# Optimization experiments

Measured on AMD Instinct MI355X. Metric: run time of the kernel, lower is better.

## Reference

```python
import jax, jax.numpy as jnp
import numpy as np

D_MODEL = 1024
H = 16
DK = D_MODEL // H
B, S = 2, 2048
NEG = -1e9


def setup_inputs() -> dict:
    key = jax.random.key(0)
    ks = jax.random.split(key, 7)
    scale = 1.0 / np.sqrt(D_MODEL)
    inp = {
        "q": jax.random.normal(ks[0], (B, S, D_MODEL), jnp.float32),
        "k": jax.random.normal(ks[1], (B, S, D_MODEL), jnp.float32),
        "v": jax.random.normal(ks[2], (B, S, D_MODEL), jnp.float32),
        # causal mask, broadcastable to (B, H, S, S); positions with 0 are masked
        "mask": jnp.tril(jnp.ones((S, S), dtype=bool))[None, None, :, :],
        "w_q": jax.random.normal(ks[3], (D_MODEL, D_MODEL), jnp.float32) * scale,
        "w_k": jax.random.normal(ks[4], (D_MODEL, D_MODEL), jnp.float32) * scale,
        "w_v": jax.random.normal(ks[5], (D_MODEL, D_MODEL), jnp.float32) * scale,
        "w_o": jax.random.normal(ks[6], (D_MODEL, D_MODEL), jnp.float32) * scale,
    }
    return inp


def reference(q, k, v, mask, w_q, w_k, w_v, w_o):
    # Linear projections (nn.Linear with bias=False: x @ W.T)
    query = q @ w_q.T  # (B, S, d_model)
    key_ = k @ w_k.T
    value = v @ w_v.T
    # split heads -> (B, h, S, dk)
    def split(x):
        return x.reshape(x.shape[0], x.shape[1], H, DK).transpose(0, 2, 1, 3)
    qh, kh, vh = split(query), split(key_), split(value)
    # scaled dot-product attention with full score materialization
    scores = jnp.einsum("bhqd,bhkd->bhqk", qh, kh) / jnp.sqrt(jnp.float32(DK))
    scores = jnp.where(mask, scores, NEG)
    attn = jax.nn.softmax(scores, axis=-1)  # (B, h, S, S); dropout p=0.0 -> identity
    out = jnp.einsum("bhqk,bhkd->bhqd", attn, vh)
    # merge heads -> (B, S, d_model)
    out = out.transpose(0, 2, 1, 3).reshape(out.shape[0], -1, H * DK)
    return out @ w_o.T
```

## Files before the change

kernel.cpp:

```cpp
#include <hip/hip_runtime.h>
#include <cstdint>
#include <cstddef>

typedef __bf16 bf16;
typedef __attribute__((ext_vector_type(4))) __bf16 bf16x4;
typedef __attribute__((ext_vector_type(8))) __bf16 bf16x8;
typedef __attribute__((ext_vector_type(4))) float floatx4;
typedef __attribute__((ext_vector_type(4))) short short4v;

#define MFMA16(a, b, c) __builtin_amdgcn_mfma_f32_16x16x32_bf16((a), (b), (c), 0, 0, 0)

__device__ __forceinline__ floatx4 MFMAK16(bf16x4 a, bf16x4 b, floatx4 c) {
#if __has_builtin(__builtin_amdgcn_mfma_f32_16x16x16bf16_1k)
  return __builtin_amdgcn_mfma_f32_16x16x16bf16_1k(
      __builtin_bit_cast(short4v, a), __builtin_bit_cast(short4v, b), c, 0, 0, 0);
#else
  floatx4 d;
  asm("v_mfma_f32_16x16x16_bf16 %0, %1, %2, %3"
      : "=v"(d)
      : "v"(a), "v"(b), "v"(c));
  return d;
#endif
}

constexpr int DMODEL = 1024;
constexpr int NH = 16;
constexpr int DKH = 64;
constexpr int B_ = 2;
constexpr int S_ = 2048;
constexpr int MTOT = B_ * S_;
constexpr float CEXP = 0.125f * 1.44269504f;

__device__ __forceinline__ void load_lds16(const void* g, void* l) {
  __builtin_amdgcn_global_load_lds(
      (const __attribute__((address_space(1))) uint32_t*)g,
      (__attribute__((address_space(3))) uint32_t*)l, 16, 0, 0);
}

__device__ __forceinline__ bf16x8 frag64(const bf16* lds, int row, int p) {
  int s = p ^ (row & 7);
  return *(const bf16x8*)&lds[row * 64 + s * 8];
}
__device__ __forceinline__ bf16x4 frag64h(const bf16* lds, int row, int p, int h) {
  int s = p ^ (row & 7);
  return *(const bf16x4*)&lds[row * 64 + s * 8 + h * 4];
}

__device__ __forceinline__ void stage32_bf16(const bf16* __restrict__ src,
                                             bf16* lds, int wave, int lane,
                                             int ldg) {
#pragma unroll
  for (int i = 0; i < 2; ++i) {
    int cb = (wave * 2 + i) * 64;
    int c = cb + lane;
    int r = c >> 2;
    int s = (c & 3) ^ ((r >> 1) & 3);
    load_lds16(&src[(size_t)r * ldg + s * 8], &lds[cb * 8]);
  }
}
__device__ __forceinline__ bf16x8 frag32_bf16(const bf16* lds, int row,
                                              int quad) {
  int s = quad ^ ((row >> 1) & 3);
  return *(const bf16x8*)&lds[row * 32 + s * 8];
}
__device__ __forceinline__ void stage32_f32(const float* __restrict__ src,
                                            float* lds, int wave, int lane,
                                            int ldg) {
#pragma unroll
  for (int i = 0; i < 4; ++i) {
    int cb = (wave * 4 + i) * 64;
    int c = cb + lane;
    int r = c >> 3;
    int s = (c & 7) ^ (r & 7);
    load_lds16(&src[(size_t)r * ldg + s * 4], &lds[cb * 4]);
  }
}
__device__ __forceinline__ bf16x8 frag32_f32(const float* lds, int row,
                                             int quad) {
  int s1 = (2 * quad) ^ (row & 7);
  int s2 = (2 * quad + 1) ^ (row & 7);
  float4 a = *(const float4*)&lds[row * 32 + s1 * 4];
  float4 b = *(const float4*)&lds[row * 32 + s2 * 4];
  bf16x8 h = {(bf16)a.x, (bf16)a.y, (bf16)a.z, (bf16)a.w,
              (bf16)b.x, (bf16)b.y, (bf16)b.z, (bf16)b.w};
  return h;
}

__global__ __launch_bounds__(256) void convert_kernel(
    const float* __restrict__ q, const float* __restrict__ k,
    const float* __restrict__ v, const float* __restrict__ wq,
    const float* __restrict__ wk, const float* __restrict__ wv,
    const float* __restrict__ wo, bf16* __restrict__ qb, bf16* __restrict__ kb,
    bf16* __restrict__ vb, bf16* __restrict__ wqb, bf16* __restrict__ wkb,
    bf16* __restrict__ wvb, bf16* __restrict__ wob) {
  const float* src;
  bf16* dst;
  size_t n;
  switch (blockIdx.y) {
    case 0: src = q;  dst = qb;  n = (size_t)MTOT * DMODEL; break;
    case 1: src = k;  dst = kb;  n = (size_t)MTOT * DMODEL; break;
    case 2: src = v;  dst = vb;  n = (size_t)MTOT * DMODEL; break;
    case 3: src = wq; dst = wqb; n = (size_t)DMODEL * DMODEL; break;
    case 4: src = wk; dst = wkb; n = (size_t)DMODEL * DMODEL; break;
    case 5: src = wv; dst = wvb; n = (size_t)DMODEL * DMODEL; break;
    default: src = wo; dst = wob; n = (size_t)DMODEL * DMODEL; break;
  }
  size_t idx = ((size_t)blockIdx.x * 256 + threadIdx.x) * 8;
  if (idx >= n) return;
  float4 f0 = *(const float4*)&src[idx];
  float4 f1 = *(const float4*)&src[idx + 4];
  bf16x8 h = {(bf16)f0.x, (bf16)f0.y, (bf16)f0.z, (bf16)f0.w,
              (bf16)f1.x, (bf16)f1.y, (bf16)f1.z, (bf16)f1.w};
  *(bf16x8*)&dst[idx] = h;
}

template <typename TC>
__device__ __forceinline__ void gemm64(const bf16* __restrict__ A,
                                       const bf16* __restrict__ W,
                                       TC* __restrict__ C,
                                       bf16* __restrict__ vt, int K,
                                       int m0, int n0, float ascale) {
  constexpr int N = DMODEL;
  __shared__ alignas(16) bf16 As[128 * 64];
  __shared__ alignas(16) bf16 Bs[128 * 64];

  const int tid = threadIdx.x;
  const int wave = tid >> 6;
  const int lane = tid & 63;
  const int quad = lane >> 4;
  const int l16 = lane & 15;
  const int wm = (wave >> 1) * 64;
  const int wn = (wave & 1) * 64;

  floatx4 acc[4][4] = {};

  for (int k0 = 0; k0 < K; k0 += 64) {
#pragma unroll
    for (int i = 0; i < 4; ++i) {
      int cb = (wave * 4 + i) * 64;
      int c = cb + lane;
      int r = c >> 3;
      int s = (c & 7) ^ (r & 7);
      load_lds16(&A[(size_t)(m0 + r) * K + k0 + s * 8], &As[cb * 8]);
      load_lds16(&W[(size_t)(n0 + r) * K + k0 + s * 8], &Bs[cb * 8]);
    }
    __syncthreads();

#pragma unroll
    for (int kk = 0; kk < 2; ++kk) {
      bf16x8 af[4], bfv[4];
#pragma unroll
      for (int mi = 0; mi < 4; ++mi)
        af[mi] = frag64(As, wm + mi * 16 + l16, kk * 4 + quad);
#pragma unroll
      for (int ni = 0; ni < 4; ++ni)
        bfv[ni] = frag64(Bs, wn + ni * 16 + l16, kk * 4 + quad);
#pragma unroll
      for (int mi = 0; mi < 4; ++mi)
#pragma unroll
        for (int ni = 0; ni < 4; ++ni)
          acc[mi][ni] = MFMA16(af[mi], bfv[ni], acc[mi][ni]);
    }
    __syncthreads();
  }

  if (vt) {
#pragma unroll
    for (int mi = 0; mi < 4; ++mi)
#pragma unroll
      for (int ni = 0; ni < 4; ++ni)
#pragma unroll
        for (int r = 0; r < 4; ++r) {
          int row = m0 + wm + mi * 16 + quad * 4 + r;
          int col = n0 + wn + ni * 16 + l16;
          int bb = row >> 11, s = row & 2047;
          int h = col >> 6, d = col & 63;
          vt[(size_t)((bb * NH + h) * DKH + d) * S_ + s] = (bf16)acc[mi][ni][r];
        }
  } else {
#pragma unroll
    for (int mi = 0; mi < 4; ++mi)
#pragma unroll
      for (int ni = 0; ni < 4; ++ni)
#pragma unroll
        for (int r = 0; r < 4; ++r) {
          int row = m0 + wm + mi * 16 + quad * 4 + r;
          int col = n0 + wn + ni * 16 + l16;
          C[(size_t)row * N + col] = (TC)(acc[mi][ni][r] * ascale);
        }
  }
}

__global__ __launch_bounds__(256, 3) void qkv64_kernel(
    const bf16* __restrict__ q, const bf16* __restrict__ k,
    const bf16* __restrict__ v, const bf16* __restrict__ wq,
    const bf16* __restrict__ wk, const bf16* __restrict__ wv,
    bf16* __restrict__ Q, bf16* __restrict__ K, bf16* __restrict__ Vt) {
  const int bid = blockIdx.x;
  const int xcd = bid & 7;
  const int j = bid >> 3;
  const int n = j & 7;
  const int rowslot = j >> 3;
  const int p = xcd * 12 + rowslot;
  const int z = p >> 5;
  const int y = p & 31;

  const bf16* A = (z == 0) ? q : (z == 1) ? k : v;
  const bf16* W = (z == 0) ? wq : (z == 1) ? wk : wv;
  bf16* C = (z == 0) ? Q : K;
  gemm64<bf16>(A, W, (z == 2) ? nullptr : C, (z == 2) ? Vt : nullptr,
               DMODEL, y * 128, n * 128, (z == 0) ? CEXP : 1.0f);
}

__global__ __launch_bounds__(256) void oproj64_kernel(
    const bf16* __restrict__ A, const bf16* __restrict__ W,
    float* __restrict__ C) {
  constexpr int K = DMODEL;
  constexpr int N = DMODEL;
  __shared__ alignas(16) bf16 As[64 * 64];
  __shared__ alignas(16) bf16 Bs[128 * 64];

  const int bid = blockIdx.x;
  const int xcd = bid & 7;
  const int j = bid >> 3;
  const int n = j & 7;
  const int slot = j >> 3;
  const int mt = xcd * 8 + slot;
  const int m0 = mt * 64;
  const int n0 = n * 128;

  const int tid = threadIdx.x;
  const int wave = tid >> 6;
  const int lane = tid & 63;
  const int quad = lane >> 4;
  const int l16 = lane & 15;
  const int wm = (wave >> 1) * 32;
  const int wn = (wave & 1) * 64;

  floatx4 acc[2][4] = {};

  for (int k0 = 0; k0 < K; k0 += 64) {
#pragma unroll
    for (int i = 0; i < 2; ++i) {
      int cb = (wave * 2 + i) * 64;
      int c = cb + lane;
      int r = c >> 3;
      int s = (c & 7) ^ (r & 7);
      load_lds16(&A[(size_t)(m0 + r) * K + k0 + s * 8], &As[cb * 8]);
    }
#pragma unroll
    for (int i = 0; i < 4; ++i) {
      int cb = (wave * 4 + i) * 64;
      int c = cb + lane;
      int r = c >> 3;
      int s = (c & 7) ^ (r & 7);
      load_lds16(&W[(size_t)(n0 + r) * K + k0 + s * 8], &Bs[cb * 8]);
    }
    __syncthreads();

#pragma unroll
    for (int kk = 0; kk < 2; ++kk) {
      bf16x8 af[2], bfv[4];
#pragma unroll
      for (int mi = 0; mi < 2; ++mi)
        af[mi] = frag64(As, wm + mi * 16 + l16, kk * 4 + quad);
#pragma unroll
      for (int ni = 0; ni < 4; ++ni)
        bfv[ni] = frag64(Bs, wn + ni * 16 + l16, kk * 4 + quad);
#pragma unroll
      for (int mi = 0; mi < 2; ++mi)
#pragma unroll
        for (int ni = 0; ni < 4; ++ni)
          acc[mi][ni] = MFMA16(af[mi], bfv[ni], acc[mi][ni]);
    }
    __syncthreads();
  }

#pragma unroll
  for (int mi = 0; mi < 2; ++mi)
#pragma unroll
    for (int ni = 0; ni < 4; ++ni)
#pragma unroll
      for (int r = 0; r < 4; ++r) {
        int row = m0 + wm + mi * 16 + quad * 4 + r;
        int col = n0 + wn + ni * 16 + l16;
        C[(size_t)row * N + col] = acc[mi][ni][r];
      }
}

template <typename TA, typename TW, typename TC>
__device__ __forceinline__ void gemm_core(const TA* __restrict__ A,
                                          const TW* __restrict__ W,
                                          TC* __restrict__ C,
                                          bf16* __restrict__ vt, int K,
                                          int m0, int n0, float ascale) {
  constexpr int N = DMODEL;
  __shared__ alignas(16) char smem[128 * 32 * (sizeof(TA) + sizeof(TW))];
  TA* As = (TA*)smem;
  TW* Bs = (TW*)(smem + 128 * 32 * sizeof(TA));

  const int tid = threadIdx.x;
  const int wave = tid >> 6;
  const int lane = tid & 63;
  const int quad = lane >> 4;
  const int l16 = lane & 15;
  const int wm = (wave >> 1) * 64;
  const int wn = (wave & 1) * 64;

  floatx4 acc[4][4] = {};

  for (int k0 = 0; k0 < K; k0 += 32) {
    if constexpr (sizeof(TA) == 2)
      stage32_bf16((const bf16*)A + (size_t)m0 * K + k0, (bf16*)As, wave, lane, K);
    else
      stage32_f32((const float*)A + (size_t)m0 * K + k0, (float*)As, wave, lane, K);
    if constexpr (sizeof(TW) == 2)
      stage32_bf16((const bf16*)W + (size_t)n0 * K + k0, (bf16*)Bs, wave, lane, K);
    else
      stage32_f32((const float*)W + (size_t)n0 * K + k0, (float*)Bs, wave, lane, K);
    __syncthreads();

    bf16x8 af[4], bfv[4];
#pragma unroll
    for (int mi = 0; mi < 4; ++mi) {
      if constexpr (sizeof(TA) == 2)
        af[mi] = frag32_bf16((const bf16*)As, wm + mi * 16 + l16, quad);
      else
        af[mi] = frag32_f32((const float*)As, wm + mi * 16 + l16, quad);
    }
#pragma unroll
    for (int ni = 0; ni < 4; ++ni) {
      if constexpr (sizeof(TW) == 2)
        bfv[ni] = frag32_bf16((const bf16*)Bs, wn + ni * 16 + l16, quad);
      else
        bfv[ni] = frag32_f32((const float*)Bs, wn + ni * 16 + l16, quad);
    }
#pragma unroll
    for (int mi = 0; mi < 4; ++mi)
#pragma unroll
      for (int ni = 0; ni < 4; ++ni)
        acc[mi][ni] = MFMA16(af[mi], bfv[ni], acc[mi][ni]);
    __syncthreads();
  }

  if (vt) {
#pragma unroll
    for (int mi = 0; mi < 4; ++mi)
#pragma unroll
      for (int ni = 0; ni < 4; ++ni)
#pragma unroll
        for (int r = 0; r < 4; ++r) {
          int row = m0 + wm + mi * 16 + quad * 4 + r;
          int col = n0 + wn + ni * 16 + l16;
          int bb = row >> 11, s = row & 2047;
          int h = col >> 6, d = col & 63;
          vt[(size_t)((bb * NH + h) * DKH + d) * S_ + s] = (bf16)acc[mi][ni][r];
        }
  } else {
#pragma unroll
    for (int mi = 0; mi < 4; ++mi)
#pragma unroll
      for (int ni = 0; ni < 4; ++ni)
#pragma unroll
        for (int r = 0; r < 4; ++r) {
          int row = m0 + wm + mi * 16 + quad * 4 + r;
          int col = n0 + wn + ni * 16 + l16;
          C[(size_t)row * N + col] = (TC)(acc[mi][ni][r] * ascale);
        }
  }
}

__global__ __launch_bounds__(256) void qkv_f32_kernel(
    const float* __restrict__ q, const float* __restrict__ k,
    const float* __restrict__ v, const float* __restrict__ wq,
    const float* __restrict__ wk, const float* __restrict__ wv,
    bf16* __restrict__ Q, bf16* __restrict__ K, bf16* __restrict__ Vt) {
  const int bid = blockIdx.x;
  const int xcd = bid & 7;
  const int j = bid >> 3;
  const int n = j & 7;
  const int rowslot = j >> 3;
  const int p = xcd * 12 + rowslot;
  const int z = p >> 5;
  const int y = p & 31;
  const float* A = (z == 0) ? q : (z == 1) ? k : v;
  const float* W = (z == 0) ? wq : (z == 1) ? wk : wv;
  bf16* C = (z == 0) ? Q : K;
  gemm_core<float, float, bf16>(A, W, (z == 2) ? nullptr : C,
                                (z == 2) ? Vt : nullptr, DMODEL, y * 128,
                                n * 128, (z == 0) ? CEXP : 1.0f);
}

__global__ __launch_bounds__(256) void oproj_f32_kernel(
    const bf16* __restrict__ A, const float* __restrict__ W,
    float* __restrict__ C) {
  const int bid = blockIdx.x;
  const int xcd = bid & 7;
  const int j = bid >> 3;
  const int n = j & 7;
  const int rowslot = j >> 3;
  const int y = xcd * 4 + rowslot;
  gemm_core<bf16, float, float>(A, W, C, nullptr, DMODEL, y * 128, n * 128,
                                1.0f);
}

__global__ __launch_bounds__(256) void attn6_kernel(const bf16* __restrict__ Q,
                                                    const bf16* __restrict__ K,
                                                    const bf16* __restrict__ Vt,
                                                    bf16* __restrict__ O) {
  __shared__ alignas(16) bf16 Ks[64 * 64];
  __shared__ alignas(16) bf16 Vts[64 * 64];

  const int tid = threadIdx.x;
  const int wave = tid >> 6;
  const int lane = tid & 63;
  const int quad = lane >> 4;
  const int l16 = lane & 15;

  const int j = blockIdx.x;
  const int qt = 31 - (j >> 5);
  const int bh = j & 31;
  const int h = bh & 15;
  const int b = bh >> 4;
  const int q0 = qt * 64;
  const size_t baseQ = (size_t)b * S_ * DMODEL + (size_t)h * DKH;
  const size_t baseV = (size_t)bh * DKH * S_;

  bf16x8 qf[2];
#pragma unroll
  for (int kk = 0; kk < 2; ++kk)
    qf[kk] = *(const bf16x8*)&Q[baseQ +
        (size_t)(q0 + wave * 16 + l16) * DMODEL + kk * 32 + quad * 8];

  floatx4 ot[4] = {};
  float lp[4] = {};
  const int qb = wave * 16 + l16;

  for (int kt = 0; kt <= qt; ++kt) {
    __syncthreads();
#pragma unroll
    for (int i = 0; i < 2; ++i) {
      int cb = (wave * 2 + i) * 64;
      int c = cb + lane;
      int r = c >> 3;
      int s = (c & 7) ^ (r & 7);
      load_lds16(&K[baseQ + (size_t)(kt * 64 + r) * DMODEL + s * 8], &Ks[cb * 8]);
      load_lds16(&Vt[baseV + (size_t)r * S_ + kt * 64 + s * 8], &Vts[cb * 8]);
    }
    __syncthreads();

    floatx4 sa[4] = {};
#pragma unroll
    for (int kk = 0; kk < 2; ++kk)
#pragma unroll
      for (int kg = 0; kg < 4; ++kg) {
        bf16x8 ka = frag64(Ks, kg * 16 + l16, kk * 4 + quad);
        sa[kg] = MFMA16(ka, qf[kk], sa[kg]);
      }

    bf16x4 pb[4];
    if (kt == qt) {
#pragma unroll
      for (int kg = 0; kg < 4; ++kg) {
        float pv[4];
#pragma unroll
        for (int r = 0; r < 4; ++r) {
          int key = kg * 16 + quad * 4 + r;
          float s = (key > qb) ? -3.0e38f : sa[kg][r];
          float p = __builtin_amdgcn_exp2f(s);
          lp[kg] += p;
          pv[r] = p;
        }
        pb[kg] = bf16x4{(bf16)pv[0], (bf16)pv[1], (bf16)pv[2], (bf16)pv[3]};
      }
    } else {
#pragma unroll
      for (int kg = 0; kg < 4; ++kg) {
        float pv[4];
#pragma unroll
        for (int r = 0; r < 4; ++r) {
          float p = __builtin_amdgcn_exp2f(sa[kg][r]);
          lp[kg] += p;
          pv[r] = p;
        }
        pb[kg] = bf16x4{(bf16)pv[0], (bf16)pv[1], (bf16)pv[2], (bf16)pv[3]};
      }
    }

#pragma unroll
    for (int kg = 0; kg < 4; ++kg)
#pragma unroll
      for (int di = 0; di < 4; ++di) {
        bf16x4 va = frag64h(Vts, di * 16 + l16, kg * 2 + (quad >> 1), quad & 1);
        ot[di] = MFMAK16(va, pb[kg], ot[di]);
      }
  }

  float l = (lp[0] + lp[1]) + (lp[2] + lp[3]);
  l += __shfl_xor(l, 16, 64);
  l += __shfl_xor(l, 32, 64);
  const float inv = 1.0f / l;

  const size_t orow = baseQ + (size_t)(q0 + wave * 16 + l16) * DMODEL;
#pragma unroll
  for (int di = 0; di < 4; ++di)
#pragma unroll
    for (int r = 0; r < 4; ++r)
      O[orow + di * 16 + quad * 4 + r] = (bf16)(ot[di][r] * inv);
}

extern "C" void kernel_launch(void* const* d_in, const int* in_sizes, int n_in,
                              void* d_out, int out_size, void* d_ws,
                              size_t ws_size, hipStream_t stream) {
  const float* q = (const float*)d_in[0];
  const float* k = (const float*)d_in[1];
  const float* v = (const float*)d_in[2];
  const float* wq = (const float*)d_in[4];
  const float* wk = (const float*)d_in[5];
  const float* wv = (const float*)d_in[6];
  const float* wo = (const float*)d_in[7];
  float* out = (float*)d_out;

  const size_t MB = 1024 * 1024;
  char* base = (char*)d_ws;
  bf16* Qp = (bf16*)(base);
  bf16* Kp = (bf16*)(base + 8 * MB);
  bf16* VtG = (bf16*)(base + 16 * MB);
  bf16* AO = (bf16*)(base + 24 * MB);

  if (ws_size >= 64 * MB) {
    bf16* qb = (bf16*)(base + 32 * MB);
    bf16* kb = (bf16*)(base + 40 * MB);
    bf16* vb = (bf16*)(base + 48 * MB);
    bf16* wqb = (bf16*)(base + 56 * MB);
    bf16* wkb = (bf16*)(base + 58 * MB);
    bf16* wvb = (bf16*)(base + 60 * MB);
    bf16* wob = (bf16*)(base + 62 * MB);
    convert_kernel<<<dim3(2048, 7), 256, 0, stream>>>(
        q, k, v, wq, wk, wv, wo, qb, kb, vb, wqb, wkb, wvb, wob);
    qkv64_kernel<<<dim3(768), 256, 0, stream>>>(
        qb, kb, vb, wqb, wkb, wvb, Qp, Kp, VtG);
    attn6_kernel<<<dim3(1024), 256, 0, stream>>>(Qp, Kp, VtG, AO);
    oproj64_kernel<<<dim3(512), 256, 0, stream>>>(AO, wob, out);
  } else {
    qkv_f32_kernel<<<dim3(768), 256, 0, stream>>>(
        q, k, v, wq, wk, wv, Qp, Kp, VtG);
    attn6_kernel<<<dim3(1024), 256, 0, stream>>>(Qp, Kp, VtG, AO);
    oproj_f32_kernel<<<dim3(256), 256, 0, stream>>>(AO, wo, out);
  }
}
```

Before: 208.6 us.

## Pair low and high causal query tiles per block with double-buffered KV

Each attention block now handles two query tiles (pr and 31-pr) of the same head, so every block does a balanced amount of causal work and shares each staged K/V tile between both. K/V staging is double-buffered, so the next tile is loaded while the current one is computed, and the MFMA section runs at raised wave priority. The grid is halved to 512 blocks, which lowers parallelism and raises register pressure from the doubled accumulators.

```diff
diff --git a/kernel.cpp b/kernel.cpp
--- a/kernel.cpp
+++ b/kernel.cpp
@@ -404,12 +404,69 @@
                                 1.0f);
 }
 
-__global__ __launch_bounds__(256) void attn6_kernel(const bf16* __restrict__ Q,
+__device__ __forceinline__ void stage_kv(const bf16* __restrict__ K,
+                                         const bf16* __restrict__ Vt,
+                                         bf16* Ks, bf16* Vts, size_t baseQ,
+                                         size_t baseV, int kt, int wave,
+                                         int lane) {
+#pragma unroll
+  for (int i = 0; i < 2; ++i) {
+    int cb = (wave * 2 + i) * 64;
+    int c = cb + lane;
+    int r = c >> 3;
+    int s = (c & 7) ^ (r & 7);
+    load_lds16(&K[baseQ + (size_t)(kt * 64 + r) * DMODEL + s * 8], &Ks[cb * 8]);
+    load_lds16(&Vt[baseV + (size_t)r * S_ + kt * 64 + s * 8], &Vts[cb * 8]);
+  }
+}
+
+template <bool DIAG>
+__device__ __forceinline__ void attn_tile(const bf16* Ks, const bf16* Vts,
+                                          const bf16x8 qf[2], floatx4 ot[4],
+                                          float lp[4], int quad, int l16,
+                                          int qb) {
+  floatx4 sa[4] = {};
+#pragma unroll
+  for (int kk = 0; kk < 2; ++kk)
+#pragma unroll
+    for (int kg = 0; kg < 4; ++kg) {
+      bf16x8 ka = frag64(Ks, kg * 16 + l16, kk * 4 + quad);
+      sa[kg] = MFMA16(ka, qf[kk], sa[kg]);
+    }
+
+  bf16x4 pb[4];
+#pragma unroll
+  for (int kg = 0; kg < 4; ++kg) {
+    float pv[4];
+#pragma unroll
+    for (int r = 0; r < 4; ++r) {
+      float s = sa[kg][r];
+      if (DIAG) {
+        int key = kg * 16 + quad * 4 + r;
+        s = (key > qb) ? -3.0e38f : s;
+      }
+      float p = __builtin_amdgcn_exp2f(s);
+      lp[kg] += p;
+      pv[r] = p;
+    }
+    pb[kg] = bf16x4{(bf16)pv[0], (bf16)pv[1], (bf16)pv[2], (bf16)pv[3]};
+  }
+
+#pragma unroll
+  for (int kg = 0; kg < 4; ++kg)
+#pragma unroll
+    for (int di = 0; di < 4; ++di) {
+      bf16x4 va = frag64h(Vts, di * 16 + l16, kg * 2 + (quad >> 1), quad & 1);
+      ot[di] = MFMAK16(va, pb[kg], ot[di]);
+    }
+}
+
+__global__ __launch_bounds__(256) void attn7_kernel(const bf16* __restrict__ Q,
                                                     const bf16* __restrict__ K,
                                                     const bf16* __restrict__ Vt,
                                                     bf16* __restrict__ O) {
-  __shared__ alignas(16) bf16 Ks[64 * 64];
-  __shared__ alignas(16) bf16 Vts[64 * 64];
+  __shared__ alignas(16) bf16 Ks[2][64 * 64];
+  __shared__ alignas(16) bf16 Vts[2][64 * 64];
 
   const int tid = threadIdx.x;
   const int wave = tid >> 6;
@@ -418,95 +475,68 @@
   const int l16 = lane & 15;
 
   const int j = blockIdx.x;
-  const int qt = 31 - (j >> 5);
   const int bh = j & 31;
+  const int pr = j >> 5;
+  const int qtL = pr;
+  const int qtH = 31 - pr;
   const int h = bh & 15;
   const int b = bh >> 4;
-  const int q0 = qt * 64;
   const size_t baseQ = (size_t)b * S_ * DMODEL + (size_t)h * DKH;
   const size_t baseV = (size_t)bh * DKH * S_;
 
-  bf16x8 qf[2];
-#pragma unroll
-  for (int kk = 0; kk < 2; ++kk)
-    qf[kk] = *(const bf16x8*)&Q[baseQ +
-        (size_t)(q0 + wave * 16 + l16) * DMODEL + kk * 32 + quad * 8];
-
-  floatx4 ot[4] = {};
-  float lp[4] = {};
+  bf16x8 qfL[2], qfH[2];
+#pragma unroll
+  for (int kk = 0; kk < 2; ++kk) {
+    qfL[kk] = *(const bf16x8*)&Q[baseQ +
+        (size_t)(qtL * 64 + wave * 16 + l16) * DMODEL + kk * 32 + quad * 8];
+    qfH[kk] = *(const bf16x8*)&Q[baseQ +
+        (size_t)(qtH * 64 + wave * 16 + l16) * DMODEL + kk * 32 + quad * 8];
+  }
+
+  floatx4 otL[4] = {}, otH[4] = {};
+  float lpL[4] = {}, lpH[4] = {};
   const int qb = wave * 16 + l16;
 
-  for (int kt = 0; kt <= qt; ++kt) {
-    __syncthreads();
-#pragma unroll
-    for (int i = 0; i < 2; ++i) {
-      int cb = (wave * 2 + i) * 64;
-      int c = cb + lane;
-      int r = c >> 3;
-      int s = (c & 7) ^ (r & 7);
-      load_lds16(&K[baseQ + (size_t)(kt * 64 + r) * DMODEL + s * 8], &Ks[cb * 8]);
-      load_lds16(&Vt[baseV + (size_t)r * S_ + kt * 64 + s * 8], &Vts[cb * 8]);
-    }
-    __syncthreads();
-
-    floatx4 sa[4] = {};
-#pragma unroll
-    for (int kk = 0; kk < 2; ++kk)
-#pragma unroll
-      for (int kg = 0; kg < 4; ++kg) {
-        bf16x8 ka = frag64(Ks, kg * 16 + l16, kk * 4 + quad);
-        sa[kg] = MFMA16(ka, qf[kk], sa[kg]);
-      }
-
-    bf16x4 pb[4];
-    if (kt == qt) {
-#pragma unroll
-      for (int kg = 0; kg < 4; ++kg) {
-        float pv[4];
-#pragma unroll
-        for (int r = 0; r < 4; ++r) {
-          int key = kg * 16 + quad * 4 + r;
-          float s = (key > qb) ? -3.0e38f : sa[kg][r];
-          float p = __builtin_amdgcn_exp2f(s);
-          lp[kg] += p;
-          pv[r] = p;
-        }
-        pb[kg] = bf16x4{(bf16)pv[0], (bf16)pv[1], (bf16)pv[2], (bf16)pv[3]};
-      }
-    } else {
-#pragma unroll
-      for (int kg = 0; kg < 4; ++kg) {
-        float pv[4];
-#pragma unroll
-        for (int r = 0; r < 4; ++r) {
-          float p = __builtin_amdgcn_exp2f(sa[kg][r]);
-          lp[kg] += p;
-          pv[r] = p;
-        }
-        pb[kg] = bf16x4{(bf16)pv[0], (bf16)pv[1], (bf16)pv[2], (bf16)pv[3]};
-      }
-    }
-
-#pragma unroll
-    for (int kg = 0; kg < 4; ++kg)
-#pragma unroll
-      for (int di = 0; di < 4; ++di) {
-        bf16x4 va = frag64h(Vts, di * 16 + l16, kg * 2 + (quad >> 1), quad & 1);
-        ot[di] = MFMAK16(va, pb[kg], ot[di]);
-      }
-  }
-
-  float l = (lp[0] + lp[1]) + (lp[2] + lp[3]);
-  l += __shfl_xor(l, 16, 64);
-  l += __shfl_xor(l, 32, 64);
-  const float inv = 1.0f / l;
-
-  const size_t orow = baseQ + (size_t)(q0 + wave * 16 + l16) * DMODEL;
+  stage_kv(K, Vt, Ks[0], Vts[0], baseQ, baseV, 0, wave, lane);
+  __syncthreads();
+
+  for (int kt = 0; kt < qtH; ++kt) {
+    const int cur = kt & 1;
+    stage_kv(K, Vt, Ks[cur ^ 1], Vts[cur ^ 1], baseQ, baseV, kt + 1, wave, lane);
+
+    __builtin_amdgcn_s_setprio(1);
+    if (kt < qtL)
+      attn_tile<false>(Ks[cur], Vts[cur], qfL, otL, lpL, quad, l16, qb);
+    else if (kt == qtL)
+      attn_tile<true>(Ks[cur], Vts[cur], qfL, otL, lpL, quad, l16, qb);
+    attn_tile<false>(Ks[cur], Vts[cur], qfH, otH, lpH, quad, l16, qb);
+    __builtin_amdgcn_s_setprio(0);
+
+    __syncthreads();
+  }
+  {
+    const int cur = qtH & 1;
+    attn_tile<true>(Ks[cur], Vts[cur], qfH, otH, lpH, quad, l16, qb);
+  }
+
+  float lL = (lpL[0] + lpL[1]) + (lpL[2] + lpL[3]);
+  lL += __shfl_xor(lL, 16, 64);
+  lL += __shfl_xor(lL, 32, 64);
+  float lH = (lpH[0] + lpH[1]) + (lpH[2] + lpH[3]);
+  lH += __shfl_xor(lH, 16, 64);
+  lH += __shfl_xor(lH, 32, 64);
+  const float invL = 1.0f / lL;
+  const float invH = 1.0f / lH;
+
+  const size_t orowL = baseQ + (size_t)(qtL * 64 + wave * 16 + l16) * DMODEL;
+  const size_t orowH = baseQ + (size_t)(qtH * 64 + wave * 16 + l16) * DMODEL;
 #pragma unroll
   for (int di = 0; di < 4; ++di)
 #pragma unroll
-    for (int r = 0; r < 4; ++r)
-      O[orow + di * 16 + quad * 4 + r] = (bf16)(ot[di][r] * inv);
+    for (int r = 0; r < 4; ++r) {
+      O[orowL + di * 16 + quad * 4 + r] = (bf16)(otL[di][r] * invL);
+      O[orowH + di * 16 + quad * 4 + r] = (bf16)(otH[di][r] * invH);
+    }
 }
 
 extern "C" void kernel_launch(void* const* d_in, const int* in_sizes, int n_in,
@@ -540,12 +570,12 @@
         q, k, v, wq, wk, wv, wo, qb, kb, vb, wqb, wkb, wvb, wob);
     qkv64_kernel<<<dim3(768), 256, 0, stream>>>(
         qb, kb, vb, wqb, wkb, wvb, Qp, Kp, VtG);
-    attn6_kernel<<<dim3(1024), 256, 0, stream>>>(Qp, Kp, VtG, AO);
+    attn7_kernel<<<dim3(512), 256, 0, stream>>>(Qp, Kp, VtG, AO);
     oproj64_kernel<<<dim3(512), 256, 0, stream>>>(AO, wob, out);
   } else {
     qkv_f32_kernel<<<dim3(768), 256, 0, stream>>>(
         q, k, v, wq, wk, wv, Qp, Kp, VtG);
-    attn6_kernel<<<dim3(1024), 256, 0, stream>>>(Qp, Kp, VtG, AO);
+    attn7_kernel<<<dim3(512), 256, 0, stream>>>(Qp, Kp, VtG, AO);
     oproj_f32_kernel<<<dim3(256), 256, 0, stream>>>(AO, wo, out);
   }
 }
```

Measured after the change: 208.2 us. Within noise of the previous version (-0.2%).
